# Optimization experiments

Measured on AMD Instinct MI355X. Metric: run time of the kernel, lower is better.

## Reference

```python
import jax, jax.numpy as jnp
import numpy as np

B, T, V, D, H = 256, 64, 6207, 512, 512  # batch, seq_len, vocab, emb_dim, hidden_dim
YF = 2048   # image feature dim -> concat with h (512) = 2560 gate input
EPS = 1e-10


def setup_inputs() -> dict:
    key = jax.random.key(0)
    ks = jax.random.split(key, 20)
    # torch init_parameters(): all params ~ U(-0.05, 0.05)
    u = lambda k, s: jax.random.uniform(k, s, jnp.float32, -0.05, 0.05)
    return {
        "y": jax.random.normal(ks[0], (B, YF), jnp.float32),
        "x": jax.random.randint(ks[1], (B, T), 0, V),
        "emb_w": u(ks[2], (V, D)),
        # bottom LSTM cell (input 512 -> hidden 512), torch layout: W_ih (4H, D)
        "W_ih": u(ks[3], (4 * H, D)), "W_hh": u(ks[4], (4 * H, H)),
        "b_ih": u(ks[5], (4 * H,)), "b_hh": u(ks[6], (4 * H,)),
        # top LSTM cell (input 512 -> hidden 512)
        "W_ih_t": u(ks[7], (4 * H, H)), "W_hh_t": u(ks[8], (4 * H, H)),
        "b_ih_t": u(ks[9], (4 * H,)), "b_hh_t": u(ks[10], (4 * H,)),
        # gate linear: Linear(2560, 512)
        "Wg": u(ks[11], (H, H + YF)), "bg": u(ks[12], (H,)),
        # final linear: Linear(512, 256)
        "Wlin": u(ks[13], (256, H)), "blin": u(ks[14], (256,)),
        # per-step gumbel-sigmoid uniforms (sampled inside forward in torch;
        # precomputed here so the reference is deterministic)
        "u1": jax.random.uniform(ks[15], (T, B, H), jnp.float32),
        "u2": jax.random.uniform(ks[16], (T, B, H), jnp.float32),
    }


def _lstm_cell(xt, h, c, Wi, Wh, bi, bh):
    # torch nn.LSTM gate order: i, f, g, o
    z = xt @ Wi.T + bi + h @ Wh.T + bh          # (B, 4H)
    i, f, g, o = jnp.split(z, 4, axis=-1)
    c = jax.nn.sigmoid(f) * c + jax.nn.sigmoid(i) * jnp.tanh(g)
    h = jax.nn.sigmoid(o) * jnp.tanh(c)
    return h, c


def reference(y, x, emb_w, W_ih, W_hh, b_ih, b_hh,
              W_ih_t, W_hh_t, b_ih_t, b_hh_t, Wg, bg, Wlin, blin, u1, u2):
    xs = jnp.transpose(emb_w[x], (1, 0, 2))     # (T, B, D)

    def step(carry, ins):
        h, c, ht, ct = carry
        xt, u1t, u2t = ins
        h, c = _lstm_cell(xt, h, c, W_ih, W_hh, b_ih, b_hh)
        # gate logits: relu(Linear([h, y]))
        logits = jax.nn.relu(jnp.concatenate([h, y], axis=1) @ Wg.T + bg)
        # custom gumbel-sigmoid noise: -log(log(U2+eps)/log(U1+eps)+eps)
        noise = -jnp.log(jnp.log(u2t + EPS) / jnp.log(u1t + EPS) + EPS)
        y_soft = jax.nn.sigmoid(logits + noise)
        # hard threshold at 0.5 with straight-through estimator
        y_hard = (y_soft >= 0.5).astype(y_soft.dtype)
        gate = y_hard - jax.lax.stop_gradient(y_soft) + y_soft
        hf = h * gate
        ht, ct = _lstm_cell(hf, ht, ct, W_ih_t, W_hh_t, b_ih_t, b_hh_t)
        return (h, c, ht, ct), None

    z0 = jnp.zeros((B, H), jnp.float32)
    (_, _, ht, _), _ = jax.lax.scan(step, (z0, z0, z0, z0), (xs, u1, u2))
    # dropout is identity in eval mode; torch output is (1, B, 256), squeezed here
    return jax.nn.relu(ht @ Wlin.T + blin)      # (B, 256)
```

## Files before the change

kernel.cpp:

```cpp
#include <hip/hip_runtime.h>
#include <hip/hip_bf16.h>


typedef __attribute__((ext_vector_type(8))) short short8;
typedef __attribute__((ext_vector_type(4))) float floatx4;
typedef __attribute__((ext_vector_type(4))) unsigned int uintx4;

#define MFMA16(a, b, c) __builtin_amdgcn_mfma_f32_16x16x32_bf16(a, b, c, 0, 0, 0)
#define AGENT __HIP_MEMORY_SCOPE_AGENT
#define HWREG_XCC_ID ((31u << 11) | (0u << 6) | 20u)

__device__ inline float bf2f(ushort u) {
    union { unsigned int u32; float f; } v; v.u32 = ((unsigned int)u) << 16; return v.f;
}
__device__ inline ushort f2bf(float f) {
    union { float f; unsigned int u; } v; v.f = f;
    return (ushort)((v.u + 0x7fffu + ((v.u >> 16) & 1u)) >> 16);
}
__device__ inline short8 ld8(const ushort* p) { return *(const short8*)p; }
__device__ inline float sigf(float x) { return 1.0f / (1.0f + expf(-x)); }
__device__ inline void mm3(floatx4& acc, short8 ah, short8 al, short8 bh, short8 bl) {
    acc = MFMA16(ah, bh, acc);
    acc = MFMA16(ah, bl, acc);
    acc = MFMA16(al, bh, acc);
}

__global__ __launch_bounds__(256) void k_prep(const float* __restrict__ w0,
                                              const float* __restrict__ w1,
                                              const float* __restrict__ w2,
                                              const float* __restrict__ w3,
                                              const float* __restrict__ wg,
                                              const float* __restrict__ wl,
                                              const float* __restrict__ em,
                                              const float* __restrict__ yy,
                                              ushort* __restrict__ wreg,
                                              uint* __restrict__ zbase) {
    unsigned i = blockIdx.x * 256u + threadIdx.x;
    if (i >= 9866784u) return;
    if (i >= 9338368u) {
        zbase[i - 9338368u] = 0u;
        return;
    }
    const float* src; ushort* hi; unsigned n, loc;
    if (i < 4194304u) {
        unsigned seg = i >> 20; loc = i & 1048575u; n = 1048576u;
        hi = wreg + seg * 2097152u;
        src = (seg == 0) ? w0 : (seg == 1) ? w1 : (seg == 2) ? w2 : w3;
    } else if (i < 5505024u) { loc = i - 4194304u; src = wg; hi = wreg + 8388608u;  n = 1310720u; }
    else if (i < 5636096u)   { loc = i - 5505024u; src = wl; hi = wreg + 11010048u; n = 131072u; }
    else if (i < 8814080u)   { loc = i - 5636096u; src = em; hi = wreg + 11272192u; n = 3177984u; }
    else                     { loc = i - 8814080u; src = yy; hi = wreg + 17628160u; n = 524288u; }
    float v = src[loc];
    ushort h = f2bf(v);
    hi[loc] = h;
    hi[n + loc] = f2bf(v - bf2f(h));
}

__global__ __launch_bounds__(512) void k_gy(const ushort* __restrict__ y_hi,
                                            const ushort* __restrict__ y_lo,
                                            const ushort* __restrict__ Wg_hi,
                                            const ushort* __restrict__ Wg_lo,
                                            const float* __restrict__ bg,
                                            float* __restrict__ gy) {
    __shared__ float zsB[4 * 528];
    int tid = threadIdx.x, lane = tid & 63, w = tid >> 6;
    int quad = lane >> 4, lr = lane & 15, q8 = quad * 8;
    int r0 = (blockIdx.x >> 4) * 16, n0 = (blockIdx.x & 15) * 32;
    int nh = w & 1, kq = w >> 1;
    int arow = r0 + lr, brow = n0 + nh * 16 + lr;
    floatx4 acc = {};
#pragma unroll
    for (int k0 = 0; k0 < 512; k0 += 32) {
        short8 ah = ld8(y_hi + arow * 2048 + kq * 512 + k0 + q8);
        short8 al = ld8(y_lo + arow * 2048 + kq * 512 + k0 + q8);
        short8 bh = ld8(Wg_hi + brow * 2560 + 512 + kq * 512 + k0 + q8);
        short8 bl = ld8(Wg_lo + brow * 2560 + 512 + kq * 512 + k0 + q8);
        mm3(acc, ah, al, bh, bl);
    }
#pragma unroll
    for (int r4 = 0; r4 < 4; r4++)
        zsB[kq * 528 + (quad * 4 + r4) * 33 + nh * 16 + lr] = acc[r4];
    __syncthreads();
    int ml = tid >> 5, jj = tid & 31;
    float s = zsB[ml * 33 + jj] + zsB[528 + ml * 33 + jj] +
              zsB[1056 + ml * 33 + jj] + zsB[1584 + ml * 33 + jj];
    gy[(r0 + ml) * 512 + n0 + jj] = s + bg[n0 + jj];
}

struct KP {
    const float *b_ih, *b_hh, *b_iht, *b_hht, *u1, *u2, *gy;
    const int* x;
    uint *hseq, *bseq, *tseq;
    uint* claim;
    uint *hP0, *hP1, *htP0, *htP1, *bitsP;
    ushort *ht_hi, *ht_lo;
    const ushort *Whh_hi, *Whh_lo, *Wih_hi, *Wih_lo;
    const ushort *Wiht_hi, *Wiht_lo, *Whht_hi, *Whht_lo;
    const ushort *Wg_hi, *Wg_lo, *em_hi, *em_lo;
};

__device__ inline void publish(uint* sq, uint v) {
    asm volatile("" ::: "memory");
    __builtin_amdgcn_s_waitcnt(0);
    __syncthreads();
    if (threadIdx.x == 0)
        __hip_atomic_store(sq, v, __ATOMIC_RELAXED, AGENT);
}
__device__ inline void poll16(const uint* sq, uint target) {
    if ((threadIdx.x >> 6) == 0) {
        int l = threadIdx.x & 63;
        for (;;) {
            uint v = (l < 16) ? __hip_atomic_load(&sq[l], __ATOMIC_RELAXED, AGENT) : target;
            if (__all((int)(v >= target))) break;
            __builtin_amdgcn_s_sleep(1);
        }
    }
    __syncthreads();
}
__device__ inline void poll_ht(const uint* hsq, const uint* tsq, uint th, uint tt) {
    if ((threadIdx.x >> 6) == 0) {
        int l = threadIdx.x & 63;
        for (;;) {
            uint v, tgt;
            if (l < 16)      { v = __hip_atomic_load(&hsq[l], __ATOMIC_RELAXED, AGENT); tgt = th; }
            else if (l < 32) { v = __hip_atomic_load(&tsq[l - 16], __ATOMIC_RELAXED, AGENT); tgt = tt; }
            else             { v = 0u; tgt = 0u; }
            if (__all((int)(v >= tgt))) break;
            __builtin_amdgcn_s_sleep(1);
        }
    }
    __syncthreads();
}

__device__ inline void issue_row16(const uint* __restrict__ src, int r0, uintx4* v) {
    int tid = threadIdx.x;
    int sr = tid >> 5, scol = (tid & 31) * 16;
    const uint* pp = src + (r0 + sr) * 512 + scol;
    asm volatile(
        "global_load_dwordx4 %0, %4, off sc0 sc1\n\t"
        "global_load_dwordx4 %1, %4, off offset:16 sc0 sc1\n\t"
        "global_load_dwordx4 %2, %4, off offset:32 sc0 sc1\n\t"
        "global_load_dwordx4 %3, %4, off offset:48 sc0 sc1"
        : "=v"(v[0]), "=v"(v[1]), "=v"(v[2]), "=v"(v[3])
        : "v"(pp) : "memory");
}
__device__ inline void unpack_row16(const uintx4* v, ushort* __restrict__ dst) {
    int tid = threadIdx.x;
    int sr = tid >> 5, scol = (tid & 31) * 16;
    ushort* d = dst + sr * 1032 + scol;
    union { uint u[4]; short8 s; } H0, H1, L0, L1;
    H0.u[0] = (v[0][0] & 0xffffu) | (v[0][1] << 16);
    H0.u[1] = (v[0][2] & 0xffffu) | (v[0][3] << 16);
    H0.u[2] = (v[1][0] & 0xffffu) | (v[1][1] << 16);
    H0.u[3] = (v[1][2] & 0xffffu) | (v[1][3] << 16);
    L0.u[0] = (v[0][0] >> 16) | (v[0][1] & 0xffff0000u);
    L0.u[1] = (v[0][2] >> 16) | (v[0][3] & 0xffff0000u);
    L0.u[2] = (v[1][0] >> 16) | (v[1][1] & 0xffff0000u);
    L0.u[3] = (v[1][2] >> 16) | (v[1][3] & 0xffff0000u);
    H1.u[0] = (v[2][0] & 0xffffu) | (v[2][1] << 16);
    H1.u[1] = (v[2][2] & 0xffffu) | (v[2][3] << 16);
    H1.u[2] = (v[3][0] & 0xffffu) | (v[3][1] << 16);
    H1.u[3] = (v[3][2] & 0xffffu) | (v[3][3] << 16);
    L1.u[0] = (v[2][0] >> 16) | (v[2][1] & 0xffff0000u);
    L1.u[1] = (v[2][2] >> 16) | (v[2][3] & 0xffff0000u);
    L1.u[2] = (v[3][0] >> 16) | (v[3][1] & 0xffff0000u);
    L1.u[3] = (v[3][2] >> 16) | (v[3][3] & 0xffff0000u);
    *(short8*)(d) = H0.s;
    *(short8*)(d + 8) = H1.s;
    *(short8*)(d + 520) = L0.s;
    *(short8*)(d + 520 + 8) = L1.s;
}

__device__ inline void stage_emb(const ushort* __restrict__ emh,
                                 const ushort* __restrict__ eml,
                                 const int* __restrict__ x, int r0, int t,
                                 ushort* __restrict__ dst) {
    int tid = threadIdx.x;
    int sr = tid >> 5, sc = (tid & 31) * 16;
    int tok = x[(r0 + sr) * 64 + t];
    const short8* ph = (const short8*)(emh + (size_t)tok * 512 + sc);
    const short8* pl = (const short8*)(eml + (size_t)tok * 512 + sc);
    short8 h0 = ph[0], h1 = ph[1], l0 = pl[0], l1 = pl[1];
    ushort* d = dst + sr * 1032;
    *(short8*)(d + sc) = h0;       *(short8*)(d + sc + 8) = h1;
    *(short8*)(d + 520 + sc) = l0; *(short8*)(d + 520 + sc + 8) = l1;
}

__device__ inline short8 fragA(const ushort* As, int row, int k) {
    return *(const short8*)(As + row * 1032 + k);
}

__device__ inline short8 mask8(uint ch) {
    union { uint u[4]; short8 s; } mk;
#pragma unroll
    for (int j = 0; j < 4; j++) {
        uint b0 = 0u - ((ch >> (2 * j)) & 1u);
        uint b1 = 0u - ((ch >> (2 * j + 1)) & 1u);
        mk.u[j] = (b0 & 0xffffu) | (b1 << 16);
    }
    return mk.s;
}

__global__ void __launch_bounds__(512, 1) k_main(KP p) {
    __shared__ ushort As[16 * 1032];
    __shared__ ushort Ae[16 * 1032];
    __shared__ ushort Az[16 * 1032];
    __shared__ float zsDA[4224];
    __shared__ float zsC1[2112];
    __shared__ float zsC2[2112];
    __shared__ uint gbitsT[256];
    __shared__ uint role_s;

    const int tid = threadIdx.x;
    const int w = tid >> 6;
    const int lane = tid & 63;
    const int quad = lane >> 4;
    const int lr = lane & 15;
    const int q8 = quad * 8;
    const float EPS = 1e-10f;

    if (tid == 0) {
        uint xcc = __builtin_amdgcn_s_getreg(HWREG_XCC_ID) & 7u;
        uint slot = __hip_atomic_fetch_add(&p.claim[xcc * 16], 1u,
                                           __ATOMIC_RELAXED, AGENT) & 31u;
        role_s = xcc * 32u + slot;
    }
    __syncthreads();
    const uint role = role_s;
    const int jb = (int)(role >> 4);
    const int g16 = (int)(role & 15u);
    const int r0 = g16 * 16, j0 = jb * 32;

    const int g4 = w & 3, team = w >> 2;
    const int gate = w >> 1, nh = w & 1;
    const int brow = gate * 512 + j0 + nh * 16 + lr;
    const int kq = w >> 1;
    const int browB = j0 + nh * 16 + lr;
    const int ml = tid >> 5, jj = tid & 31;

    const float biasAe0 = p.b_ih[j0 + jj]        + p.b_hh[j0 + jj];
    const float biasAe1 = p.b_ih[512 + j0 + jj]  + p.b_hh[512 + j0 + jj];
    const float biasAe2 = p.b_ih[1024 + j0 + jj] + p.b_hh[1024 + j0 + jj];
    const float biasAe3 = p.b_ih[1536 + j0 + jj] + p.b_hh[1536 + j0 + jj];
    const float biasCe0 = p.b_iht[j0 + jj]        + p.b_hht[j0 + jj];
    const float biasCe1 = p.b_iht[512 + j0 + jj]  + p.b_hht[512 + j0 + jj];
    const float biasCe2 = p.b_iht[1024 + j0 + jj] + p.b_hht[1024 + j0 + jj];
    const float biasCe3 = p.b_iht[1536 + j0 + jj] + p.b_hht[1536 + j0 + jj];
    const float gy_r = p.gy[(r0 + ml) * 512 + j0 + jj];

    const int rowA = g4 * 512 + j0 + lr;
    const ushort* WAh = (team ? p.Wih_hi : p.Whh_hi) + rowA * 512;
    const ushort* WAl = (team ? p.Wih_lo : p.Whh_lo) + rowA * 512;
    const ushort* WitH = p.Wiht_hi + brow * 512;
    const ushort* WitL = p.Wiht_lo + brow * 512;
    const ushort* WgH = p.Wg_hi + browB * 2560 + kq * 128;
    const ushort* WgL = p.Wg_lo + browB * 2560 + kq * 128;
    const float* pu1 = p.u1 + (r0 + ml) * 512 + j0 + jj;
    const float* pu2 = p.u2 + (r0 + ml) * 512 + j0 + jj;
    uint* hs = p.hseq + g16 * 16;
    uint* bs = p.bseq + g16 * 16;
    uint* hts = p.tseq + g16 * 16;

    short8 wHt[16], wLt[16];
    {
        const ushort* WhtH = p.Whht_hi + brow * 512;
        const ushort* WhtL = p.Whht_lo + brow * 512;
#pragma unroll
        for (int kk = 0; kk < 16; kk++) {
            wHt[kk] = ld8(WhtH + kk * 32 + q8);
            wLt[kk] = ld8(WhtL + kk * 32 + q8);
        }
    }

    for (int i = tid; i < 16 * 1032; i += 512) As[i] = 0;
    stage_emb(p.em_hi, p.em_lo, p.x, r0, 0, Ae);
    float U1 = __builtin_nontemporal_load(pu1);
    float U2 = __builtin_nontemporal_load(pu2);
    __syncthreads();

    float c_reg = 0.0f, ct_reg = 0.0f;

    for (int t = 0; t < 64; t++) {
        {
            const ushort* Ax = team ? Ae : As;
            floatx4 acc0 = {}, acc1 = {};
#pragma unroll
            for (int k0 = 0; k0 < 512; k0 += 32) {
                short8 xh = fragA(Ax, lr, k0 + q8);
                short8 xl = fragA(Ax, lr, 520 + k0 + q8);
                mm3(acc0, xh, xl, ld8(WAh + k0 + q8), ld8(WAl + k0 + q8));
                mm3(acc1, xh, xl, ld8(WAh + 8192 + k0 + q8), ld8(WAl + 8192 + k0 + q8));
            }
#pragma unroll
            for (int r4 = 0; r4 < 4; r4++) {
                zsDA[team * 2112 + (quad * 4 + r4) * 132 + g4 * 32 + lr]      = acc0[r4];
                zsDA[team * 2112 + (quad * 4 + r4) * 132 + g4 * 32 + 16 + lr] = acc1[r4];
            }
        }
        __syncthreads();
        uint* hPcur = (t & 1) ? p.hP1 : p.hP0;
        {
            float zi = (zsDA[ml * 132 + jj]      + zsDA[2112 + ml * 132 + jj])      + biasAe0;
            float zf = (zsDA[ml * 132 + 32 + jj] + zsDA[2112 + ml * 132 + 32 + jj]) + biasAe1;
            float zg = (zsDA[ml * 132 + 64 + jj] + zsDA[2112 + ml * 132 + 64 + jj]) + biasAe2;
            float zo = (zsDA[ml * 132 + 96 + jj] + zsDA[2112 + ml * 132 + 96 + jj]) + biasAe3;
            c_reg = sigf(zf) * c_reg + sigf(zi) * tanhf(zg);
            float hv = sigf(zo) * tanhf(c_reg);
            ushort hb = f2bf(hv);
            ushort lb = f2bf(hv - bf2f(hb));
            __hip_atomic_store(&hPcur[(r0 + ml) * 512 + j0 + jj],
                               (uint)hb | ((uint)lb << 16), __ATOMIC_RELAXED, AGENT);
        }
        if (t > 0) {
            floatx4 c1acc = {};
#pragma unroll
            for (int kk = 0; kk < 16; kk++) {
                uint word = gbitsT[kk * 16 + lr];
                short8 mk = mask8((word >> q8) & 0xffu);
                short8 ah = fragA(As, lr, kk * 32 + q8) & mk;
                short8 al = fragA(As, lr, 520 + kk * 32 + q8) & mk;
                mm3(c1acc, ah, al, ld8(WitH + kk * 32 + q8), ld8(WitL + kk * 32 + q8));
            }
#pragma unroll
            for (int r4 = 0; r4 < 4; r4++)
                zsC1[(quad * 4 + r4) * 132 + gate * 32 + nh * 16 + lr] = c1acc[r4];
        }
        __syncthreads();
        if (t > 0) {
            float zi = (zsC1[ml * 132 + jj]      + zsC2[ml * 132 + jj])      + biasCe0;
            float zf = (zsC1[ml * 132 + 32 + jj] + zsC2[ml * 132 + 32 + jj]) + biasCe1;
            float zg = (zsC1[ml * 132 + 64 + jj] + zsC2[ml * 132 + 64 + jj]) + biasCe2;
            float zo = (zsC1[ml * 132 + 96 + jj] + zsC2[ml * 132 + 96 + jj]) + biasCe3;
            ct_reg = sigf(zf) * ct_reg + sigf(zi) * tanhf(zg);
            float hv = sigf(zo) * tanhf(ct_reg);
            ushort hb = f2bf(hv);
            ushort lb = f2bf(hv - bf2f(hb));
            uint* htcur = (t & 1) ? p.htP0 : p.htP1;
            __hip_atomic_store(&htcur[(r0 + ml) * 512 + j0 + jj],
                               (uint)hb | ((uint)lb << 16), __ATOMIC_RELAXED, AGENT);
        }
        asm volatile("s_waitcnt vmcnt(0)" ::: "memory");
        __builtin_amdgcn_sched_barrier(0);
        __syncthreads();
        if (tid == 0) {
            __hip_atomic_store(&hs[jb], (uint)(t + 1), __ATOMIC_RELAXED, AGENT);
            __hip_atomic_store(&hts[jb], (uint)t, __ATOMIC_RELAXED, AGENT);
        }
        float noise = -logf(logf(U2 + EPS) / logf(U1 + EPS) + EPS);
        poll_ht(hs, hts, (uint)(t + 1), (uint)t);
        uintx4 va[4], vz[4];
        issue_row16(hPcur, r0, va);
        issue_row16((t & 1) ? p.htP0 : p.htP1, r0, vz);
        asm volatile("s_waitcnt vmcnt(0)" ::: "memory");
        __builtin_amdgcn_sched_barrier(0);
        unpack_row16(va, As);
        unpack_row16(vz, Az);
        __syncthreads();
        {
            floatx4 acc = {};
#pragma unroll
            for (int k0 = 0; k0 < 128; k0 += 32)
                mm3(acc, fragA(As, lr, kq * 128 + k0 + q8),
                    fragA(As, lr, 520 + kq * 128 + k0 + q8),
                    ld8(WgH + k0 + q8), ld8(WgL + k0 + q8));
#pragma unroll
            for (int r4 = 0; r4 < 4; r4++)
                zsDA[kq * 528 + (quad * 4 + r4) * 33 + nh * 16 + lr] = acc[r4];
        }
        __syncthreads();
        {
            float z2 = zsDA[ml * 33 + jj] + zsDA[528 + ml * 33 + jj] +
                       zsDA[1056 + ml * 33 + jj] + zsDA[1584 + ml * 33 + jj];
            float logit = fmaxf(z2 + gy_r, 0.0f);
            bool gbit = sigf(logit + noise) >= 0.5f;
            unsigned long long bm = __ballot((int)gbit);
            if ((lane & 31) == 0)
                __hip_atomic_store(&p.bitsP[(r0 + ml) * 16 + jb],
                                   (uint)(bm >> ((lane >> 5) * 32)),
                                   __ATOMIC_RELAXED, AGENT);
        }
        publish(&bs[jb], (uint)(t + 1));
        if (t < 63) stage_emb(p.em_hi, p.em_lo, p.x, r0, t + 1, Ae);
        {
            floatx4 c2acc = {};
#pragma unroll
            for (int kk = 0; kk < 16; kk++)
                mm3(c2acc, fragA(Az, lr, kk * 32 + q8),
                    fragA(Az, lr, 520 + kk * 32 + q8), wHt[kk], wLt[kk]);
#pragma unroll
            for (int r4 = 0; r4 < 4; r4++)
                zsC2[(quad * 4 + r4) * 132 + gate * 32 + nh * 16 + lr] = c2acc[r4];
        }
        poll16(bs, (uint)(t + 1));
        uint rb = 0;
        if (tid < 256)
            asm volatile("global_load_dword %0, %1, off sc0 sc1"
                         : "=v"(rb) : "v"(p.bitsP + r0 * 16 + tid) : "memory");
        if (t < 63) {
            U1 = __builtin_nontemporal_load(pu1 + (t + 1) * 131072);
            U2 = __builtin_nontemporal_load(pu2 + (t + 1) * 131072);
            asm volatile("s_waitcnt vmcnt(2)" ::: "memory");
        } else {
            asm volatile("s_waitcnt vmcnt(0)" ::: "memory");
        }
        __builtin_amdgcn_sched_barrier(0);
        if (tid < 256) gbitsT[(tid & 15) * 16 + (tid >> 4)] = rb;
        __syncthreads();
    }
    {
        floatx4 c1acc = {};
#pragma unroll
        for (int kk = 0; kk < 16; kk++) {
            uint word = gbitsT[kk * 16 + lr];
            short8 mk = mask8((word >> q8) & 0xffu);
            short8 ah = fragA(As, lr, kk * 32 + q8) & mk;
            short8 al = fragA(As, lr, 520 + kk * 32 + q8) & mk;
            mm3(c1acc, ah, al, ld8(WitH + kk * 32 + q8), ld8(WitL + kk * 32 + q8));
        }
#pragma unroll
        for (int r4 = 0; r4 < 4; r4++)
            zsC1[(quad * 4 + r4) * 132 + gate * 32 + nh * 16 + lr] = c1acc[r4];
    }
    __syncthreads();
    {
        float zi = (zsC1[ml * 132 + jj]      + zsC2[ml * 132 + jj])      + biasCe0;
        float zf = (zsC1[ml * 132 + 32 + jj] + zsC2[ml * 132 + 32 + jj]) + biasCe1;
        float zg = (zsC1[ml * 132 + 64 + jj] + zsC2[ml * 132 + 64 + jj]) + biasCe2;
        float zo = (zsC1[ml * 132 + 96 + jj] + zsC2[ml * 132 + 96 + jj]) + biasCe3;
        ct_reg = sigf(zf) * ct_reg + sigf(zi) * tanhf(zg);
        float hv = sigf(zo) * tanhf(ct_reg);
        ushort hb = f2bf(hv);
        ushort lb = f2bf(hv - bf2f(hb));
        int idx = (r0 + ml) * 512 + j0 + jj;
        p.ht_hi[idx] = hb; p.ht_lo[idx] = lb;
    }
}

__global__ __launch_bounds__(256) void k_final(const ushort* __restrict__ ht_hi,
                                               const ushort* __restrict__ ht_lo,
                                               const ushort* __restrict__ Wl_hi,
                                               const ushort* __restrict__ Wl_lo,
                                               const float* __restrict__ blin,
                                               float* __restrict__ out) {
    int tid = threadIdx.x, lane = tid & 63, w = tid >> 6;
    int wm = w & 1, wn = w >> 1, quad = lane >> 4, lr = lane & 15;
    int m0 = blockIdx.y * 64, n0 = blockIdx.x * 64;
    floatx4 acc[2][2] = {};
    for (int k0 = 0; k0 < 512; k0 += 32) {
        short8 ah[2], al[2], bh[2], bl[2];
#pragma unroll
        for (int tn = 0; tn < 2; tn++) {
            int n = n0 + wn * 32 + tn * 16 + lr;
            bh[tn] = ld8(Wl_hi + n * 512 + k0 + quad * 8);
            bl[tn] = ld8(Wl_lo + n * 512 + k0 + quad * 8);
        }
#pragma unroll
        for (int tm = 0; tm < 2; tm++) {
            int r = m0 + wm * 32 + tm * 16 + lr;
            ah[tm] = ld8(ht_hi + r * 512 + k0 + quad * 8);
            al[tm] = ld8(ht_lo + r * 512 + k0 + quad * 8);
        }
#pragma unroll
        for (int tm = 0; tm < 2; tm++)
#pragma unroll
            for (int tn = 0; tn < 2; tn++) mm3(acc[tm][tn], ah[tm], al[tm], bh[tn], bl[tn]);
    }
#pragma unroll
    for (int tm = 0; tm < 2; tm++)
#pragma unroll
        for (int tn = 0; tn < 2; tn++)
#pragma unroll
            for (int r4 = 0; r4 < 4; r4++) {
                int row = m0 + wm * 32 + tm * 16 + quad * 4 + r4;
                int n = n0 + wn * 32 + tn * 16 + lr;
                out[row * 256 + n] = fmaxf(acc[tm][tn][r4] + blin[n], 0.0f);
            }
}

extern "C" void kernel_launch(void* const* d_in, const int* in_sizes, int n_in,
                              void* d_out, int out_size, void* d_ws, size_t ws_size,
                              hipStream_t stream) {
    (void)in_sizes; (void)n_in; (void)out_size; (void)ws_size;
    const float* y      = (const float*)d_in[0];
    const int*   x      = (const int*)d_in[1];
    const float* emb    = (const float*)d_in[2];
    const float* W_ih   = (const float*)d_in[3];
    const float* W_hh   = (const float*)d_in[4];
    const float* b_ih   = (const float*)d_in[5];
    const float* b_hh   = (const float*)d_in[6];
    const float* W_iht  = (const float*)d_in[7];
    const float* W_hht  = (const float*)d_in[8];
    const float* b_iht  = (const float*)d_in[9];
    const float* b_hht  = (const float*)d_in[10];
    const float* Wg     = (const float*)d_in[11];
    const float* bg     = (const float*)d_in[12];
    const float* Wlin   = (const float*)d_in[13];
    const float* blin   = (const float*)d_in[14];
    const float* u1     = (const float*)d_in[15];
    const float* u2     = (const float*)d_in[16];
    float* out = (float*)d_out;

    uint* bar  = (uint*)d_ws;
    uint* hP0  = bar + 4128;
    uint* hP1  = hP0 + 131072;
    uint* htP0 = hP1 + 131072;
    uint* htP1 = htP0 + 131072;
    float* gy  = (float*)(htP1 + 131072);
    ushort* ht_hi = (ushort*)(gy + 131072);
    ushort* ht_lo = ht_hi + 131072;
    uint* bitsP = (uint*)(ht_lo + 131072);
    ushort* wreg = (ushort*)(bitsP + 4096);

    KP p;
    p.b_ih = b_ih; p.b_hh = b_hh; p.b_iht = b_iht; p.b_hht = b_hht;
    p.u1 = u1; p.u2 = u2; p.gy = gy; p.x = x;
    p.hseq = bar; p.bseq = bar + 256; p.tseq = bar + 512; p.claim = bar + 1024;
    p.hP0 = hP0; p.hP1 = hP1; p.htP0 = htP0; p.htP1 = htP1; p.bitsP = bitsP;
    p.ht_hi = ht_hi; p.ht_lo = ht_lo;
    p.Wih_hi  = wreg;             p.Wih_lo  = wreg + 1048576;
    p.Whh_hi  = wreg + 2097152;   p.Whh_lo  = wreg + 3145728;
    p.Wiht_hi = wreg + 4194304;   p.Wiht_lo = wreg + 5242880;
    p.Whht_hi = wreg + 6291456;   p.Whht_lo = wreg + 7340032;
    p.Wg_hi   = wreg + 8388608;   p.Wg_lo   = wreg + 9699328;
    p.em_hi   = wreg + 11272192;  p.em_lo   = wreg + 14450176;
    const ushort* Wl_hi = wreg + 11010048; const ushort* Wl_lo = wreg + 11141120;
    const ushort* y_hi  = wreg + 17628160; const ushort* y_lo  = wreg + 18152448;

    k_prep<<<dim3(38543), dim3(256), 0, stream>>>(W_ih, W_hh, W_iht, W_hht, Wg, Wlin,
                                                  emb, y, wreg, bar);
    k_gy<<<dim3(256), dim3(512), 0, stream>>>(y_hi, y_lo, p.Wg_hi, p.Wg_lo, bg, gy);

    void* args[] = {(void*)&p};
    hipLaunchCooperativeKernel((const void*)k_main, dim3(256), dim3(512), args, 0, stream);

    k_final<<<dim3(4, 4), dim3(256), 0, stream>>>(ht_hi, ht_lo, Wl_hi, Wl_lo, blin, out);
}
```

Measured before the change: 2.308 ms.

## Software-pipeline the three recurrent stages across timesteps with skewed sync flags

Restructures the persistent cooperative kernel so the bottom LSTM (A), the gate logits (B) and the top LSTM (C) for different timesteps run in one skewed loop of 66 iterations, with C lagging A by two steps. Top-hidden and gate-bit buffers become triple-buffered, and each sequence flag gets its own cache line so pollers do not contend. The aim is to take the gate and top-LSTM work off the critical inter-block synchronisation path of the bottom recurrence, so fewer global barriers sit on each step's latency chain. In exchange it adds more workspace, more flag memory and extra pipeline fill and drain iterations, with subtle ordering risks in the flag protocol.

New measurement: 2.266 ms. About the same (-1.8%).

```diff
diff --git a/kernel.cpp b/kernel.cpp
--- a/kernel.cpp
+++ b/kernel.cpp
@@ -36,7 +36,7 @@
                                               ushort* __restrict__ wreg,
                                               uint* __restrict__ zbase) {
     unsigned i = blockIdx.x * 256u + threadIdx.x;
-    if (i >= 9866784u) return;
+    if (i >= 10006272u) return;
     if (i >= 9338368u) {
         zbase[i - 9338368u] = 0u;
         return;
@@ -92,40 +92,40 @@
     const int* x;
     uint *hseq, *bseq, *tseq;
     uint* claim;
-    uint *hP0, *hP1, *htP0, *htP1, *bitsP;
+    uint *hP0, *hP1, *htP0, *htP1, *htP2, *bitsP;
     ushort *ht_hi, *ht_lo;
     const ushort *Whh_hi, *Whh_lo, *Wih_hi, *Wih_lo;
     const ushort *Wiht_hi, *Wiht_lo, *Whht_hi, *Whht_lo;
     const ushort *Wg_hi, *Wg_lo, *em_hi, *em_lo;
 };
 
-__device__ inline void publish(uint* sq, uint v) {
-    asm volatile("" ::: "memory");
-    __builtin_amdgcn_s_waitcnt(0);
-    __syncthreads();
-    if (threadIdx.x == 0)
-        __hip_atomic_store(sq, v, __ATOMIC_RELAXED, AGENT);
-}
-__device__ inline void poll16(const uint* sq, uint target) {
+__device__ inline void pollS(const uint* sq, int g16, uint target) {
     if ((threadIdx.x >> 6) == 0) {
         int l = threadIdx.x & 63;
         for (;;) {
-            uint v = (l < 16) ? __hip_atomic_load(&sq[l], __ATOMIC_RELAXED, AGENT) : target;
+            uint v = target;
+            if (l < 16)
+                v = __hip_atomic_load(sq + (l * 256 + g16 * 16), __ATOMIC_RELAXED, AGENT);
             if (__all((int)(v >= target))) break;
             __builtin_amdgcn_s_sleep(1);
         }
     }
     __syncthreads();
 }
-__device__ inline void poll_ht(const uint* hsq, const uint* tsq, uint th, uint tt) {
+__device__ inline void pollS2(const uint* s1, const uint* s2, int g16,
+                              uint t1, uint t2) {
     if ((threadIdx.x >> 6) == 0) {
         int l = threadIdx.x & 63;
         for (;;) {
-            uint v, tgt;
-            if (l < 16)      { v = __hip_atomic_load(&hsq[l], __ATOMIC_RELAXED, AGENT); tgt = th; }
-            else if (l < 32) { v = __hip_atomic_load(&tsq[l - 16], __ATOMIC_RELAXED, AGENT); tgt = tt; }
-            else             { v = 0u; tgt = 0u; }
-            if (__all((int)(v >= tgt))) break;
+            uint v = 0u, tg = 0u;
+            if (l < 16) {
+                v = __hip_atomic_load(s1 + (l * 256 + g16 * 16), __ATOMIC_RELAXED, AGENT);
+                tg = t1;
+            } else if (l < 32) {
+                v = __hip_atomic_load(s2 + ((l - 16) * 256 + g16 * 16), __ATOMIC_RELAXED, AGENT);
+                tg = t2;
+            }
+            if (__all((int)(v >= tg))) break;
             __builtin_amdgcn_s_sleep(1);
         }
     }
@@ -201,13 +201,17 @@
     return mk.s;
 }
 
+__device__ inline uint* sel3(uint* a, uint* b, uint* c, int s) {
+    return (s == 0) ? a : ((s == 1) ? b : c);
+}
+
 __global__ void __launch_bounds__(512, 1) k_main(KP p) {
-    __shared__ ushort As[16 * 1032];
+    __shared__ ushort Hb0[16 * 1032];
+    __shared__ ushort Hb1[16 * 1032];
     __shared__ ushort Ae[16 * 1032];
     __shared__ ushort Az[16 * 1032];
-    __shared__ float zsDA[4224];
-    __shared__ float zsC1[2112];
-    __shared__ float zsC2[2112];
+    __shared__ float zs1[2112];
+    __shared__ float zs2[2112];
     __shared__ uint gbitsT[256];
     __shared__ uint role_s;
 
@@ -257,9 +261,10 @@
     const ushort* WgL = p.Wg_lo + browB * 2560 + kq * 128;
     const float* pu1 = p.u1 + (r0 + ml) * 512 + j0 + jj;
     const float* pu2 = p.u2 + (r0 + ml) * 512 + j0 + jj;
-    uint* hs = p.hseq + g16 * 16;
-    uint* bs = p.bseq + g16 * 16;
-    uint* hts = p.tseq + g16 * 16;
+    const int fline = (jb * 16 + g16) * 16;
+    uint* myHs = p.hseq + fline;
+    uint* myBs = p.bseq + fline;
+    uint* myTs = p.tseq + fline;
 
     short8 wHt[16], wLt[16];
     {
@@ -272,17 +277,23 @@
         }
     }
 
-    for (int i = tid; i < 16 * 1032; i += 512) As[i] = 0;
+    for (int i = tid; i < 16 * 1032; i += 512) Hb1[i] = 0;
     stage_emb(p.em_hi, p.em_lo, p.x, r0, 0, Ae);
-    float U1 = __builtin_nontemporal_load(pu1);
-    float U2 = __builtin_nontemporal_load(pu2);
     __syncthreads();
 
     float c_reg = 0.0f, ct_reg = 0.0f;
-
-    for (int t = 0; t < 64; t++) {
-        {
-            const ushort* Ax = team ? Ae : As;
+    float U1n = 0.0f, U2n = 0.0f;
+
+    for (int t = 0; t < 66; t++) {
+        const bool doA = (t < 64);
+        const bool doB = (t >= 1 && t < 65);
+        const bool doC = (t >= 2);
+        ushort* Hprev = (t & 1) ? Hb0 : Hb1;
+        ushort* Hold  = (t & 1) ? Hb1 : Hb0;
+        uint* hPcur = (t & 1) ? p.hP1 : p.hP0;
+
+        if (doA) {
+            const ushort* Ax = team ? Ae : Hprev;
             floatx4 acc0 = {}, acc1 = {};
 #pragma unroll
             for (int k0 = 0; k0 < 512; k0 += 32) {
@@ -291,148 +302,134 @@
                 mm3(acc0, xh, xl, ld8(WAh + k0 + q8), ld8(WAl + k0 + q8));
                 mm3(acc1, xh, xl, ld8(WAh + 8192 + k0 + q8), ld8(WAl + 8192 + k0 + q8));
             }
+            float* zt = team ? zs2 : zs1;
 #pragma unroll
             for (int r4 = 0; r4 < 4; r4++) {
-                zsDA[team * 2112 + (quad * 4 + r4) * 132 + g4 * 32 + lr]      = acc0[r4];
-                zsDA[team * 2112 + (quad * 4 + r4) * 132 + g4 * 32 + 16 + lr] = acc1[r4];
+                zt[(quad * 4 + r4) * 132 + g4 * 32 + lr]      = acc0[r4];
+                zt[(quad * 4 + r4) * 132 + g4 * 32 + 16 + lr] = acc1[r4];
             }
         }
         __syncthreads();
-        uint* hPcur = (t & 1) ? p.hP1 : p.hP0;
-        {
-            float zi = (zsDA[ml * 132 + jj]      + zsDA[2112 + ml * 132 + jj])      + biasAe0;
-            float zf = (zsDA[ml * 132 + 32 + jj] + zsDA[2112 + ml * 132 + 32 + jj]) + biasAe1;
-            float zg = (zsDA[ml * 132 + 64 + jj] + zsDA[2112 + ml * 132 + 64 + jj]) + biasAe2;
-            float zo = (zsDA[ml * 132 + 96 + jj] + zsDA[2112 + ml * 132 + 96 + jj]) + biasAe3;
+        if (doA) {
+            float zi = (zs1[ml * 132 + jj]      + zs2[ml * 132 + jj])      + biasAe0;
+            float zf = (zs1[ml * 132 + 32 + jj] + zs2[ml * 132 + 32 + jj]) + biasAe1;
+            float zg = (zs1[ml * 132 + 64 + jj] + zs2[ml * 132 + 64 + jj]) + biasAe2;
+            float zo = (zs1[ml * 132 + 96 + jj] + zs2[ml * 132 + 96 + jj]) + biasAe3;
             c_reg = sigf(zf) * c_reg + sigf(zi) * tanhf(zg);
             float hv = sigf(zo) * tanhf(c_reg);
             ushort hb = f2bf(hv);
             ushort lb = f2bf(hv - bf2f(hb));
             __hip_atomic_store(&hPcur[(r0 + ml) * 512 + j0 + jj],
                                (uint)hb | ((uint)lb << 16), __ATOMIC_RELAXED, AGENT);
-        }
-        if (t > 0) {
+            asm volatile("s_waitcnt vmcnt(0)" ::: "memory");
+            __builtin_amdgcn_sched_barrier(0);
+        }
+        __syncthreads();
+        if (doA && tid == 0)
+            __hip_atomic_store(myHs, (uint)(t + 1), __ATOMIC_RELAXED, AGENT);
+
+        uintx4 vz[4]; uint rb = 0;
+        if (doC) {
+            pollS2(p.bseq, p.tseq, g16, (uint)(t - 1), (uint)(t - 2));
+            const uint* bsrc = sel3(p.bitsP, p.bitsP + 4096, p.bitsP + 8192,
+                                    (t + 1) % 3);
+            if (tid < 256)
+                asm volatile("global_load_dword %0, %1, off sc0 sc1"
+                             : "=v"(rb) : "v"(bsrc + r0 * 16 + tid) : "memory");
+            issue_row16(sel3(p.htP0, p.htP1, p.htP2, t % 3), r0, vz);
+        }
+        if (doB) {
+            floatx4 acc = {};
+#pragma unroll
+            for (int k0 = 0; k0 < 128; k0 += 32)
+                mm3(acc, fragA(Hprev, lr, kq * 128 + k0 + q8),
+                    fragA(Hprev, lr, 520 + kq * 128 + k0 + q8),
+                    ld8(WgH + k0 + q8), ld8(WgL + k0 + q8));
+#pragma unroll
+            for (int r4 = 0; r4 < 4; r4++)
+                zs1[kq * 528 + (quad * 4 + r4) * 33 + nh * 16 + lr] = acc[r4];
+        }
+        __syncthreads();
+        if (doB) {
+            float z2 = zs1[ml * 33 + jj] + zs1[528 + ml * 33 + jj] +
+                       zs1[1056 + ml * 33 + jj] + zs1[1584 + ml * 33 + jj];
+            float logit = fmaxf(z2 + gy_r, 0.0f);
+            float noise = -logf(logf(U2n + EPS) / logf(U1n + EPS) + EPS);
+            bool gbit = sigf(logit + noise) >= 0.5f;
+            unsigned long long bm = __ballot((int)gbit);
+            uint* bdst = sel3(p.bitsP, p.bitsP + 4096, p.bitsP + 8192,
+                              (t + 2) % 3);
+            if ((lane & 31) == 0)
+                __hip_atomic_store(&bdst[(r0 + ml) * 16 + jb],
+                                   (uint)(bm >> ((lane >> 5) * 32)),
+                                   __ATOMIC_RELAXED, AGENT);
+        }
+        asm volatile("s_waitcnt vmcnt(0)" ::: "memory");
+        __builtin_amdgcn_sched_barrier(0);
+        if (doC) {
+            unpack_row16(vz, Az);
+            if (tid < 256) gbitsT[(tid & 15) * 16 + (tid >> 4)] = rb;
+        }
+        __syncthreads();
+        if (doB && tid == 0)
+            __hip_atomic_store(myBs, (uint)t, __ATOMIC_RELAXED, AGENT);
+
+        if (doC) {
             floatx4 c1acc = {};
 #pragma unroll
             for (int kk = 0; kk < 16; kk++) {
                 uint word = gbitsT[kk * 16 + lr];
                 short8 mk = mask8((word >> q8) & 0xffu);
-                short8 ah = fragA(As, lr, kk * 32 + q8) & mk;
-                short8 al = fragA(As, lr, 520 + kk * 32 + q8) & mk;
+                short8 ah = fragA(Hold, lr, kk * 32 + q8) & mk;
+                short8 al = fragA(Hold, lr, 520 + kk * 32 + q8) & mk;
                 mm3(c1acc, ah, al, ld8(WitH + kk * 32 + q8), ld8(WitL + kk * 32 + q8));
             }
 #pragma unroll
             for (int r4 = 0; r4 < 4; r4++)
-                zsC1[(quad * 4 + r4) * 132 + gate * 32 + nh * 16 + lr] = c1acc[r4];
-        }
-        __syncthreads();
-        if (t > 0) {
-            float zi = (zsC1[ml * 132 + jj]      + zsC2[ml * 132 + jj])      + biasCe0;
-            float zf = (zsC1[ml * 132 + 32 + jj] + zsC2[ml * 132 + 32 + jj]) + biasCe1;
-            float zg = (zsC1[ml * 132 + 64 + jj] + zsC2[ml * 132 + 64 + jj]) + biasCe2;
-            float zo = (zsC1[ml * 132 + 96 + jj] + zsC2[ml * 132 + 96 + jj]) + biasCe3;
+                zs1[(quad * 4 + r4) * 132 + gate * 32 + nh * 16 + lr] = c1acc[r4];
+            floatx4 c2acc = {};
+#pragma unroll
+            for (int kk = 0; kk < 16; kk++)
+                mm3(c2acc, fragA(Az, lr, kk * 32 + q8),
+                    fragA(Az, lr, 520 + kk * 32 + q8), wHt[kk], wLt[kk]);
+#pragma unroll
+            for (int r4 = 0; r4 < 4; r4++)
+                zs2[(quad * 4 + r4) * 132 + gate * 32 + nh * 16 + lr] = c2acc[r4];
+        }
+        __syncthreads();
+        if (doC) {
+            float zi = (zs1[ml * 132 + jj]      + zs2[ml * 132 + jj])      + biasCe0;
+            float zf = (zs1[ml * 132 + 32 + jj] + zs2[ml * 132 + 32 + jj]) + biasCe1;
+            float zg = (zs1[ml * 132 + 64 + jj] + zs2[ml * 132 + 64 + jj]) + biasCe2;
+            float zo = (zs1[ml * 132 + 96 + jj] + zs2[ml * 132 + 96 + jj]) + biasCe3;
             ct_reg = sigf(zf) * ct_reg + sigf(zi) * tanhf(zg);
             float hv = sigf(zo) * tanhf(ct_reg);
             ushort hb = f2bf(hv);
             ushort lb = f2bf(hv - bf2f(hb));
-            uint* htcur = (t & 1) ? p.htP0 : p.htP1;
-            __hip_atomic_store(&htcur[(r0 + ml) * 512 + j0 + jj],
-                               (uint)hb | ((uint)lb << 16), __ATOMIC_RELAXED, AGENT);
-        }
-        asm volatile("s_waitcnt vmcnt(0)" ::: "memory");
-        __builtin_amdgcn_sched_barrier(0);
-        __syncthreads();
-        if (tid == 0) {
-            __hip_atomic_store(&hs[jb], (uint)(t + 1), __ATOMIC_RELAXED, AGENT);
-            __hip_atomic_store(&hts[jb], (uint)t, __ATOMIC_RELAXED, AGENT);
-        }
-        float noise = -logf(logf(U2 + EPS) / logf(U1 + EPS) + EPS);
-        poll_ht(hs, hts, (uint)(t + 1), (uint)t);
-        uintx4 va[4], vz[4];
-        issue_row16(hPcur, r0, va);
-        issue_row16((t & 1) ? p.htP0 : p.htP1, r0, vz);
-        asm volatile("s_waitcnt vmcnt(0)" ::: "memory");
-        __builtin_amdgcn_sched_barrier(0);
-        unpack_row16(va, As);
-        unpack_row16(vz, Az);
-        __syncthreads();
-        {
-            floatx4 acc = {};
-#pragma unroll
-            for (int k0 = 0; k0 < 128; k0 += 32)
-                mm3(acc, fragA(As, lr, kq * 128 + k0 + q8),
-                    fragA(As, lr, 520 + kq * 128 + k0 + q8),
-                    ld8(WgH + k0 + q8), ld8(WgL + k0 + q8));
-#pragma unroll
-            for (int r4 = 0; r4 < 4; r4++)
-                zsDA[kq * 528 + (quad * 4 + r4) * 33 + nh * 16 + lr] = acc[r4];
-        }
-        __syncthreads();
-        {
-            float z2 = zsDA[ml * 33 + jj] + zsDA[528 + ml * 33 + jj] +
-                       zsDA[1056 + ml * 33 + jj] + zsDA[1584 + ml * 33 + jj];
-            float logit = fmaxf(z2 + gy_r, 0.0f);
-            bool gbit = sigf(logit + noise) >= 0.5f;
-            unsigned long long bm = __ballot((int)gbit);
-            if ((lane & 31) == 0)
-                __hip_atomic_store(&p.bitsP[(r0 + ml) * 16 + jb],
-                                   (uint)(bm >> ((lane >> 5) * 32)),
-                                   __ATOMIC_RELAXED, AGENT);
-        }
-        publish(&bs[jb], (uint)(t + 1));
+            uint* tdst = sel3(p.htP0, p.htP1, p.htP2, (t + 1) % 3);
+            int idx = (r0 + ml) * 512 + j0 + jj;
+            __hip_atomic_store(&tdst[idx], (uint)hb | ((uint)lb << 16),
+                               __ATOMIC_RELAXED, AGENT);
+            if (t == 65) { p.ht_hi[idx] = hb; p.ht_lo[idx] = lb; }
+            asm volatile("s_waitcnt vmcnt(0)" ::: "memory");
+            __builtin_amdgcn_sched_barrier(0);
+        }
+        __syncthreads();
+        if (doC && tid == 0)
+            __hip_atomic_store(myTs, (uint)(t - 1), __ATOMIC_RELAXED, AGENT);
+
         if (t < 63) stage_emb(p.em_hi, p.em_lo, p.x, r0, t + 1, Ae);
-        {
-            floatx4 c2acc = {};
-#pragma unroll
-            for (int kk = 0; kk < 16; kk++)
-                mm3(c2acc, fragA(Az, lr, kk * 32 + q8),
-                    fragA(Az, lr, 520 + kk * 32 + q8), wHt[kk], wLt[kk]);
-#pragma unroll
-            for (int r4 = 0; r4 < 4; r4++)
-                zsC2[(quad * 4 + r4) * 132 + gate * 32 + nh * 16 + lr] = c2acc[r4];
-        }
-        poll16(bs, (uint)(t + 1));
-        uint rb = 0;
-        if (tid < 256)
-            asm volatile("global_load_dword %0, %1, off sc0 sc1"
-                         : "=v"(rb) : "v"(p.bitsP + r0 * 16 + tid) : "memory");
-        if (t < 63) {
-            U1 = __builtin_nontemporal_load(pu1 + (t + 1) * 131072);
-            U2 = __builtin_nontemporal_load(pu2 + (t + 1) * 131072);
+        if (doA) {
+            pollS(p.hseq, g16, (uint)(t + 1));
+            uintx4 va[4];
+            issue_row16(hPcur, r0, va);
+            U1n = __builtin_nontemporal_load(pu1 + t * 131072);
+            U2n = __builtin_nontemporal_load(pu2 + t * 131072);
             asm volatile("s_waitcnt vmcnt(2)" ::: "memory");
-        } else {
-            asm volatile("s_waitcnt vmcnt(0)" ::: "memory");
-        }
-        __builtin_amdgcn_sched_barrier(0);
-        if (tid < 256) gbitsT[(tid & 15) * 16 + (tid >> 4)] = rb;
-        __syncthreads();
-    }
-    {
-        floatx4 c1acc = {};
-#pragma unroll
-        for (int kk = 0; kk < 16; kk++) {
-            uint word = gbitsT[kk * 16 + lr];
-            short8 mk = mask8((word >> q8) & 0xffu);
-            short8 ah = fragA(As, lr, kk * 32 + q8) & mk;
-            short8 al = fragA(As, lr, 520 + kk * 32 + q8) & mk;
-            mm3(c1acc, ah, al, ld8(WitH + kk * 32 + q8), ld8(WitL + kk * 32 + q8));
-        }
-#pragma unroll
-        for (int r4 = 0; r4 < 4; r4++)
-            zsC1[(quad * 4 + r4) * 132 + gate * 32 + nh * 16 + lr] = c1acc[r4];
-    }
-    __syncthreads();
-    {
-        float zi = (zsC1[ml * 132 + jj]      + zsC2[ml * 132 + jj])      + biasCe0;
-        float zf = (zsC1[ml * 132 + 32 + jj] + zsC2[ml * 132 + 32 + jj]) + biasCe1;
-        float zg = (zsC1[ml * 132 + 64 + jj] + zsC2[ml * 132 + 64 + jj]) + biasCe2;
-        float zo = (zsC1[ml * 132 + 96 + jj] + zsC2[ml * 132 + 96 + jj]) + biasCe3;
-        ct_reg = sigf(zf) * ct_reg + sigf(zi) * tanhf(zg);
-        float hv = sigf(zo) * tanhf(ct_reg);
-        ushort hb = f2bf(hv);
-        ushort lb = f2bf(hv - bf2f(hb));
-        int idx = (r0 + ml) * 512 + j0 + jj;
-        p.ht_hi[idx] = hb; p.ht_lo[idx] = lb;
+            __builtin_amdgcn_sched_barrier(0);
+            unpack_row16(va, Hold);
+        }
+        __syncthreads();
     }
 }
 
@@ -501,21 +498,23 @@
     float* out = (float*)d_out;
 
     uint* bar  = (uint*)d_ws;
-    uint* hP0  = bar + 4128;
+    uint* hP0  = bar + 12544;
     uint* hP1  = hP0 + 131072;
     uint* htP0 = hP1 + 131072;
     uint* htP1 = htP0 + 131072;
-    float* gy  = (float*)(htP1 + 131072);
+    uint* htP2 = htP1 + 131072;
+    float* gy  = (float*)(htP2 + 131072);
     ushort* ht_hi = (ushort*)(gy + 131072);
     ushort* ht_lo = ht_hi + 131072;
     uint* bitsP = (uint*)(ht_lo + 131072);
-    ushort* wreg = (ushort*)(bitsP + 4096);
+    ushort* wreg = (ushort*)(bitsP + 12288);
 
     KP p;
     p.b_ih = b_ih; p.b_hh = b_hh; p.b_iht = b_iht; p.b_hht = b_hht;
     p.u1 = u1; p.u2 = u2; p.gy = gy; p.x = x;
-    p.hseq = bar; p.bseq = bar + 256; p.tseq = bar + 512; p.claim = bar + 1024;
-    p.hP0 = hP0; p.hP1 = hP1; p.htP0 = htP0; p.htP1 = htP1; p.bitsP = bitsP;
+    p.hseq = bar; p.bseq = bar + 4096; p.tseq = bar + 8192; p.claim = bar + 12288;
+    p.hP0 = hP0; p.hP1 = hP1; p.htP0 = htP0; p.htP1 = htP1; p.htP2 = htP2;
+    p.bitsP = bitsP;
     p.ht_hi = ht_hi; p.ht_lo = ht_lo;
     p.Wih_hi  = wreg;             p.Wih_lo  = wreg + 1048576;
     p.Whh_hi  = wreg + 2097152;   p.Whh_lo  = wreg + 3145728;
@@ -526,7 +525,7 @@
     const ushort* Wl_hi = wreg + 11010048; const ushort* Wl_lo = wreg + 11141120;
     const ushort* y_hi  = wreg + 17628160; const ushort* y_lo  = wreg + 18152448;
 
-    k_prep<<<dim3(38543), dim3(256), 0, stream>>>(W_ih, W_hh, W_iht, W_hht, Wg, Wlin,
+    k_prep<<<dim3(39087), dim3(256), 0, stream>>>(W_ih, W_hh, W_iht, W_hht, Wg, Wlin,
                                                   emb, y, wreg, bar);
     k_gy<<<dim3(256), dim3(512), 0, stream>>>(y_hi, y_lo, p.Wg_hi, p.Wg_lo, bg, gy);
 
```
